# Kernel optimization log

Measured on AMD Instinct MI355X. Metric: run time of the kernel, lower is better.

Reference implementation:

```python
import math
import jax, jax.numpy as jnp
import numpy as np

D = 1024        # latent_dim
H = 16          # num latent heads
HD = D // H     # head dim = 64
T_EMB = 9       # max(diffusion_steps+1, 2)
CLIP = 1.0      # latent_update_clip
LN_EPS = 1e-5


def layer_norm(x, g, b):
    m = jnp.mean(x, axis=-1, keepdims=True)
    v = jnp.mean(jnp.square(x - m), axis=-1, keepdims=True)
    return (x - m) * jax.lax.rsqrt(v + LN_EPS) * g + b


def setup_inputs() -> dict:
    key = jax.random.key(0)
    ks = jax.random.split(key, 10)
    B, S = 64, 64
    s = 0.02
    return {
        "latents": jax.random.normal(ks[0], (B, S, D), jnp.float32),
        "t_table": jax.random.normal(ks[1], (T_EMB, D), jnp.float32) * s,
        "attn_g": jnp.ones((D,), jnp.float32),
        "attn_b": jnp.zeros((D,), jnp.float32),
        "ffn_g": jnp.ones((D,), jnp.float32),
        "ffn_b": jnp.zeros((D,), jnp.float32),
        "Wq": jax.random.normal(ks[2], (D, D), jnp.float32) * s,
        "Wk": jax.random.normal(ks[3], (D, D), jnp.float32) * s,
        "Wv": jax.random.normal(ks[4], (D, D), jnp.float32) * s,
        "Wo": jax.random.normal(ks[5], (D, D), jnp.float32) * s,
        "Win": jax.random.normal(ks[6], (2 * D, D), jnp.float32) * s,
        "b_in": jnp.zeros((2 * D,), jnp.float32),
        "Wout": jax.random.normal(ks[7], (D, 2 * D), jnp.float32) * s,
        "b_out": jnp.zeros((D,), jnp.float32),
        "steps": 8,
    }


def _slot_attention(x, Wq, Wk, Wv, Wo):
    B, S, _ = x.shape
    scale = 1.0 / math.sqrt(HD)
    # torch Linear: y = x @ W.T ; weights stored (out, in)
    q = (x @ Wq.T).reshape(B, S, H, HD)
    k = (x @ Wk.T).reshape(B, S, H, HD)
    v = (x @ Wv.T).reshape(B, S, H, HD)
    scores = jnp.einsum("bqhd,bkhd->bhqk", q, k) * scale
    probs = jax.nn.softmax(scores, axis=-1)
    out = jnp.einsum("bhqk,bkhd->bqhd", probs, v).reshape(B, S, D)
    return out @ Wo.T


def reference(latents, t_table, attn_g, attn_b, ffn_g, ffn_b,
              Wq, Wk, Wv, Wo, Win, b_in, Wout, b_out, steps):
    h = latents
    for step in range(steps):
        step_id = min(step, T_EMB - 1)
        t_emb = t_table[step_id][None, None, :]          # [1,1,D]
        attn_update = _slot_attention(layer_norm(h + t_emb, attn_g, attn_b),
                                      Wq, Wk, Wv, Wo)
        ffn_in = layer_norm(h + t_emb + attn_update, ffn_g, ffn_b)
        ffn_update = jax.nn.silu(ffn_in @ Win.T + b_in) @ Wout.T + b_out
        update = attn_update + ffn_update
        unorm = jnp.maximum(jnp.linalg.norm(update, axis=-1, keepdims=True), 1e-6)
        update = update * jnp.minimum(CLIP / unorm, 1.0)
        h = h + update / steps
    return h
```

## Files before the change

kernel.cpp:

```cpp
#include <hip/hip_runtime.h>
#include <hip/hip_bf16.h>

typedef __attribute__((ext_vector_type(8))) short bf16x8;
typedef __attribute__((ext_vector_type(4))) float f32x4;
typedef __attribute__((ext_vector_type(4))) int i32x4;

static __device__ __forceinline__ short f2bf(float f) {
    __hip_bfloat16 h = __float2bfloat16(f);
    return __builtin_bit_cast(short, h);
}
static __device__ __forceinline__ float bf2f(short s) {
    unsigned u = ((unsigned)(unsigned short)s) << 16;
    return __builtin_bit_cast(float, u);
}

static __device__ __forceinline__ void gload_lds16(const short* g, short* l) {
    __builtin_amdgcn_global_load_lds((const __attribute__((address_space(1))) void*)g,
                                     (__attribute__((address_space(3))) void*)l, 16, 0, 0);
}

__global__ void convert_all_kernel(
    const float* __restrict__ Wq, const float* __restrict__ Wk, const float* __restrict__ Wv,
    const float* __restrict__ Wo, const float* __restrict__ Win, const float* __restrict__ Wout,
    short* __restrict__ wQKV, short* __restrict__ wO, short* __restrict__ wIn, short* __restrict__ wOut)
{
    const int M1 = 1024 * 1024;
    for (int i = blockIdx.x * blockDim.x + threadIdx.x; i < 8 * M1; i += gridDim.x * blockDim.x) {
        if (i < 3 * M1) {
            float v = (i < M1) ? Wq[i] : (i < 2 * M1) ? Wk[i - M1] : Wv[i - 2 * M1];
            wQKV[i] = f2bf(v);
        } else if (i < 4 * M1) {
            wO[i - 3 * M1] = f2bf(Wo[i - 3 * M1]);
        } else if (i < 6 * M1) {
            wIn[i - 4 * M1] = f2bf(Win[i - 4 * M1]);
        } else {
            wOut[i - 6 * M1] = f2bf(Wout[i - 6 * M1]);
        }
    }
}

__global__ __launch_bounds__(256) void first_ln_kernel(
    const float* __restrict__ latents, float* __restrict__ h,
    const float* __restrict__ trow,
    const float* __restrict__ g, const float* __restrict__ bb,
    short* __restrict__ out)
{
    const int row = blockIdx.x;
    const int tid = threadIdx.x;
    const int lane = tid & 63;
    const int wid = tid >> 6;
    __shared__ float red[4];
    const float* hr = latents + (size_t)row * 1024;
    float x[4];
    float s = 0.f;
    #pragma unroll
    for (int i = 0; i < 4; ++i) {
        int c = tid + i * 256;
        float hv = hr[c];
        h[(size_t)row * 1024 + c] = hv;
        x[i] = hv + trow[c]; s += x[i];
    }
    #pragma unroll
    for (int o = 32; o >= 1; o >>= 1) s += __shfl_xor(s, o, 64);
    if (lane == 0) red[wid] = s;
    __syncthreads();
    float mean = (red[0] + red[1] + red[2] + red[3]) * (1.0f / 1024.0f);
    __syncthreads();
    float s2 = 0.f;
    #pragma unroll
    for (int i = 0; i < 4; ++i) { float d = x[i] - mean; s2 += d * d; }
    #pragma unroll
    for (int o = 32; o >= 1; o >>= 1) s2 += __shfl_xor(s2, o, 64);
    if (lane == 0) red[wid] = s2;
    __syncthreads();
    float var = (red[0] + red[1] + red[2] + red[3]) * (1.0f / 1024.0f);
    float rstd = rsqrtf(var + 1e-5f);
    #pragma unroll
    for (int i = 0; i < 4; ++i) {
        int c = tid + i * 256;
        out[(size_t)row * 1024 + c] = f2bf((x[i] - mean) * rstd * g[c] + bb[c]);
    }
}

__global__ __launch_bounds__(256) void ln_kernel(
    const float* __restrict__ hsrc, const float* __restrict__ trow,
    const short* __restrict__ add,
    const float* __restrict__ g, const float* __restrict__ bb,
    short* __restrict__ out)
{
    const int row = blockIdx.x;
    const int tid = threadIdx.x;
    const int lane = tid & 63;
    const int wid = tid >> 6;
    __shared__ float red[4];
    const float* hr = hsrc + (size_t)row * 1024;
    float x[4];
    float s = 0.f;
    #pragma unroll
    for (int i = 0; i < 4; ++i) {
        int c = tid + i * 256;
        float v = hr[c] + trow[c];
        if (add) v += bf2f(add[(size_t)row * 1024 + c]);
        x[i] = v; s += v;
    }
    #pragma unroll
    for (int o = 32; o >= 1; o >>= 1) s += __shfl_xor(s, o, 64);
    if (lane == 0) red[wid] = s;
    __syncthreads();
    float mean = (red[0] + red[1] + red[2] + red[3]) * (1.0f / 1024.0f);
    __syncthreads();
    float s2 = 0.f;
    #pragma unroll
    for (int i = 0; i < 4; ++i) { float d = x[i] - mean; s2 += d * d; }
    #pragma unroll
    for (int o = 32; o >= 1; o >>= 1) s2 += __shfl_xor(s2, o, 64);
    if (lane == 0) red[wid] = s2;
    __syncthreads();
    float var = (red[0] + red[1] + red[2] + red[3]) * (1.0f / 1024.0f);
    float rstd = rsqrtf(var + 1e-5f);
    #pragma unroll
    for (int i = 0; i < 4; ++i) {
        int c = tid + i * 256;
        out[(size_t)row * 1024 + c] = f2bf((x[i] - mean) * rstd * g[c] + bb[c]);
    }
}

__global__ __launch_bounds__(256) void clipln_kernel(
    const short* __restrict__ upd, float* __restrict__ h,
    const float* __restrict__ trow,
    const float* __restrict__ g, const float* __restrict__ bb,
    short* __restrict__ out)
{
    const int row = blockIdx.x;
    const int tid = threadIdx.x;
    const int lane = tid & 63;
    const int wid = tid >> 6;
    __shared__ float red[4];
    const short* ur = upd + (size_t)row * 1024;
    float u[4], hn[4];
    float s = 0.f;
    #pragma unroll
    for (int i = 0; i < 4; ++i) { u[i] = bf2f(ur[tid + i * 256]); s += u[i] * u[i]; }
    #pragma unroll
    for (int o = 32; o >= 1; o >>= 1) s += __shfl_xor(s, o, 64);
    if (lane == 0) red[wid] = s;
    __syncthreads();
    float nrm = sqrtf(red[0] + red[1] + red[2] + red[3]);
    float scale = fminf(1.0f / fmaxf(nrm, 1e-6f), 1.0f) * 0.125f;
    __syncthreads();
    float sm = 0.f;
    #pragma unroll
    for (int i = 0; i < 4; ++i) {
        int c = tid + i * 256;
        hn[i] = h[(size_t)row * 1024 + c] + u[i] * scale;
        h[(size_t)row * 1024 + c] = hn[i];
        hn[i] += trow[c];
        sm += hn[i];
    }
    #pragma unroll
    for (int o = 32; o >= 1; o >>= 1) sm += __shfl_xor(sm, o, 64);
    if (lane == 0) red[wid] = sm;
    __syncthreads();
    float mean = (red[0] + red[1] + red[2] + red[3]) * (1.0f / 1024.0f);
    __syncthreads();
    float s2 = 0.f;
    #pragma unroll
    for (int i = 0; i < 4; ++i) { float d = hn[i] - mean; s2 += d * d; }
    #pragma unroll
    for (int o = 32; o >= 1; o >>= 1) s2 += __shfl_xor(s2, o, 64);
    if (lane == 0) red[wid] = s2;
    __syncthreads();
    float var = (red[0] + red[1] + red[2] + red[3]) * (1.0f / 1024.0f);
    float rstd = rsqrtf(var + 1e-5f);
    #pragma unroll
    for (int i = 0; i < 4; ++i) {
        int c = tid + i * 256;
        out[(size_t)row * 1024 + c] = f2bf((hn[i] - mean) * rstd * g[c] + bb[c]);
    }
}

template<int BM, int ACT, int ADD, int BIAS>
__global__ __launch_bounds__(512) void gemm_kernel(
    const short* __restrict__ A, const short* __restrict__ B,
    const float* __restrict__ bias, const short* __restrict__ addsrc,
    short* __restrict__ Cout, int M, int N, int K)
{
    const int nwg = gridDim.x * gridDim.y;
    const int orig = blockIdx.y * gridDim.x + blockIdx.x;
    const int swzid = (orig & 7) * (nwg >> 3) + (orig >> 3);
    const int bn = (swzid % gridDim.x) * 128;
    const int bm = (swzid / gridDim.x) * BM;

    __shared__ __align__(16) short As[BM * 64];
    __shared__ __align__(16) short Bs[128 * 64];
    const int tid = threadIdx.x;
    const int lane = tid & 63;
    const int wid = tid >> 6;
    const int l15 = lane & 15;
    const int l4 = lane >> 4;

    constexpr int MF = 2;
    constexpr int NF = (BM == 128) ? 4 : 2;
    const int rowbase = (BM == 128) ? (wid >> 1) * 32 : (wid >> 2) * 32;
    const int colbase = (BM == 128) ? (wid & 1) * 64 : (wid & 3) * 32;

    constexpr int ALOADS = BM * 8 / 512;

    f32x4 acc[MF][NF];
    #pragma unroll
    for (int m = 0; m < MF; ++m)
        #pragma unroll
        for (int n = 0; n < NF; ++n)
            acc[m][n] = (f32x4)(0.f);

    const int nt = K >> 6;
    for (int t = 0; t < nt; ++t) {
        const int k0 = t << 6;
        #pragma unroll
        for (int i = 0; i < ALOADS; ++i) {
            int slot = i * 512 + tid;
            int row = slot >> 3;
            int colb = (slot & 7) * 16;
            int swz = (row & 7) << 4;
            const short* g = A + (size_t)(bm + row) * K + k0 + ((colb ^ swz) >> 1);
            gload_lds16(g, (short*)((char*)As + slot * 16));
        }
        #pragma unroll
        for (int i = 0; i < 2; ++i) {
            int slot = i * 512 + tid;
            int row = slot >> 3;
            int colb = (slot & 7) * 16;
            int swz = (row & 7) << 4;
            const short* g = B + (size_t)(bn + row) * K + k0 + ((colb ^ swz) >> 1);
            gload_lds16(g, (short*)((char*)Bs + slot * 16));
        }
        __syncthreads();
        #pragma unroll
        for (int ks = 0; ks < 2; ++ks) {
            int kb = ks * 64 + l4 * 16;
            bf16x8 a[MF], b[NF];
            #pragma unroll
            for (int m = 0; m < MF; ++m) {
                int row = rowbase + m * 16 + l15;
                a[m] = *(const bf16x8*)((const char*)As + row * 128 + (kb ^ ((row & 7) << 4)));
            }
            #pragma unroll
            for (int n = 0; n < NF; ++n) {
                int row = colbase + n * 16 + l15;
                b[n] = *(const bf16x8*)((const char*)Bs + row * 128 + (kb ^ ((row & 7) << 4)));
            }
            #pragma unroll
            for (int m = 0; m < MF; ++m)
                #pragma unroll
                for (int n = 0; n < NF; ++n)
                    acc[m][n] = __builtin_amdgcn_mfma_f32_16x16x32_bf16(a[m], b[n], acc[m][n], 0, 0, 0);
        }
        __syncthreads();
    }

    #pragma unroll
    for (int m = 0; m < MF; ++m) {
        int row = bm + rowbase + m * 16 + l4 * 4;
        #pragma unroll
        for (int n = 0; n < NF; ++n) {
            int col = bn + colbase + n * 16 + l15;
            float bv = BIAS ? bias[col] : 0.f;
            #pragma unroll
            for (int r = 0; r < 4; ++r) {
                float v = acc[m][n][r] + bv;
                if (ACT) v = v / (1.f + __expf(-v));
                if (ADD) v += bf2f(addsrc[(size_t)(row + r) * N + col]);
                Cout[(size_t)(row + r) * N + col] = f2bf(v);
            }
        }
    }
}

__global__ __launch_bounds__(256) void attn_kernel(
    const short* __restrict__ qkv,
    short* __restrict__ ctx)
{
    const int blk = blockIdx.x;
    const int b = blk >> 4, hh = blk & 15;
    const int bs0 = b * 64;
    __shared__ __align__(16) short qs[64 * 64];
    __shared__ __align__(16) short ks_[64 * 64];
    __shared__ __align__(16) short vt[64 * 64];
    __shared__ __align__(16) short ps[64 * 64];
    const int tid = threadIdx.x;
    const int lane = tid & 63;
    const int wid = tid >> 6;
    const int l15 = lane & 15;
    const int l4 = lane >> 4;

    #pragma unroll
    for (int i = 0; i < 2; ++i) {
        int slot = i * 256 + tid;
        int row = slot >> 3;
        int colb = (slot & 7) * 16;
        int swz = (row & 7) << 4;
        const short* gq = qkv + (size_t)(bs0 + row) * 3072 + hh * 64 + (slot & 7) * 8;
        *(i32x4*)((char*)qs + row * 128 + (colb ^ swz)) = *(const i32x4*)gq;
        const short* gk = qkv + (size_t)(bs0 + row) * 3072 + 1024 + hh * 64 + (slot & 7) * 8;
        *(i32x4*)((char*)ks_ + row * 128 + (colb ^ swz)) = *(const i32x4*)gk;
        const short* gv = qkv + (size_t)(bs0 + row) * 3072 + 2048 + hh * 64 + (slot & 7) * 8;
        i32x4 vv = *(const i32x4*)gv;
        const short* ve = (const short*)&vv;
        #pragma unroll
        for (int j = 0; j < 8; ++j) {
            int d = (slot & 7) * 8 + j;
            *(short*)((char*)vt + d * 128 + ((row * 2) ^ ((d & 7) << 4))) = ve[j];
        }
    }
    __syncthreads();

    f32x4 sc[4];
    #pragma unroll
    for (int n = 0; n < 4; ++n) sc[n] = (f32x4)(0.f);
    #pragma unroll
    for (int ksz = 0; ksz < 2; ++ksz) {
        int kb = ksz * 64 + l4 * 16;
        int arow = wid * 16 + l15;
        bf16x8 af = *(const bf16x8*)((const char*)qs + arow * 128 + (kb ^ ((arow & 7) << 4)));
        #pragma unroll
        for (int n = 0; n < 4; ++n) {
            int brow = n * 16 + l15;
            bf16x8 bf = *(const bf16x8*)((const char*)ks_ + brow * 128 + (kb ^ ((brow & 7) << 4)));
            sc[n] = __builtin_amdgcn_mfma_f32_16x16x32_bf16(af, bf, sc[n], 0, 0, 0);
        }
    }
    float sm[4];
    #pragma unroll
    for (int r = 0; r < 4; ++r) {
        float m = -1e30f;
        #pragma unroll
        for (int n = 0; n < 4; ++n) { sc[n][r] *= 0.125f; m = fmaxf(m, sc[n][r]); }
        #pragma unroll
        for (int o = 1; o < 16; o <<= 1) m = fmaxf(m, __shfl_xor(m, o, 64));
        float s = 0.f;
        #pragma unroll
        for (int n = 0; n < 4; ++n) { sc[n][r] = __expf(sc[n][r] - m); s += sc[n][r]; }
        #pragma unroll
        for (int o = 1; o < 16; o <<= 1) s += __shfl_xor(s, o, 64);
        sm[r] = 1.f / s;
    }
    #pragma unroll
    for (int n = 0; n < 4; ++n)
        #pragma unroll
        for (int r = 0; r < 4; ++r) {
            int row = wid * 16 + l4 * 4 + r;
            int col = n * 16 + l15;
            *(short*)((char*)ps + row * 128 + ((col * 2) ^ ((row & 7) << 4))) = f2bf(sc[n][r] * sm[r]);
        }
    __syncthreads();

    f32x4 o[4];
    #pragma unroll
    for (int n = 0; n < 4; ++n) o[n] = (f32x4)(0.f);
    #pragma unroll
    for (int ksz = 0; ksz < 2; ++ksz) {
        int kb = ksz * 64 + l4 * 16;
        int arow = wid * 16 + l15;
        bf16x8 af = *(const bf16x8*)((const char*)ps + arow * 128 + (kb ^ ((arow & 7) << 4)));
        #pragma unroll
        for (int n = 0; n < 4; ++n) {
            int vrow = n * 16 + l15;
            bf16x8 bf = *(const bf16x8*)((const char*)vt + vrow * 128 + (kb ^ ((vrow & 7) << 4)));
            o[n] = __builtin_amdgcn_mfma_f32_16x16x32_bf16(af, bf, o[n], 0, 0, 0);
        }
    }
    #pragma unroll
    for (int n = 0; n < 4; ++n)
        #pragma unroll
        for (int r = 0; r < 4; ++r) {
            int row = wid * 16 + l4 * 4 + r;
            int col = n * 16 + l15;
            ctx[(size_t)(bs0 + row) * 1024 + hh * 64 + col] = f2bf(o[n][r]);
        }
}

__global__ __launch_bounds__(256) void clip_kernel(const short* __restrict__ upd, float* __restrict__ h) {
    const int row = blockIdx.x;
    const int tid = threadIdx.x;
    const int lane = tid & 63;
    const int wid = tid >> 6;
    __shared__ float red[4];
    const short* ur = upd + (size_t)row * 1024;
    float x[4];
    float s = 0.f;
    #pragma unroll
    for (int i = 0; i < 4; ++i) { x[i] = bf2f(ur[tid + i * 256]); s += x[i] * x[i]; }
    #pragma unroll
    for (int o = 32; o >= 1; o >>= 1) s += __shfl_xor(s, o, 64);
    if (lane == 0) red[wid] = s;
    __syncthreads();
    float nrm = sqrtf(red[0] + red[1] + red[2] + red[3]);
    float unorm = fmaxf(nrm, 1e-6f);
    float scale = fminf(1.0f / unorm, 1.0f) * 0.125f;
    #pragma unroll
    for (int i = 0; i < 4; ++i) {
        int c = tid + i * 256;
        h[(size_t)row * 1024 + c] += x[i] * scale;
    }
}

extern "C" void kernel_launch(void* const* d_in, const int* in_sizes, int n_in,
                              void* d_out, int out_size, void* d_ws, size_t ws_size,
                              hipStream_t stream) {
    const float* latents = (const float*)d_in[0];
    const float* t_table = (const float*)d_in[1];
    const float* attn_g  = (const float*)d_in[2];
    const float* attn_b  = (const float*)d_in[3];
    const float* ffn_g   = (const float*)d_in[4];
    const float* ffn_b   = (const float*)d_in[5];
    const float* Wq      = (const float*)d_in[6];
    const float* Wk      = (const float*)d_in[7];
    const float* Wv      = (const float*)d_in[8];
    const float* Wo      = (const float*)d_in[9];
    const float* Win     = (const float*)d_in[10];
    const float* b_in    = (const float*)d_in[11];
    const float* Wout    = (const float*)d_in[12];
    const float* b_out   = (const float*)d_in[13];

    char* ws = (char*)d_ws;
    size_t off = 0;
    auto alloc = [&](size_t bytes) { char* p = ws + off; off += (bytes + 255) & ~(size_t)255; return p; };
    short* wQKV = (short*)alloc((size_t)3072 * 1024 * 2);
    short* wO   = (short*)alloc((size_t)1024 * 1024 * 2);
    short* wIn  = (short*)alloc((size_t)2048 * 1024 * 2);
    short* wOut = (short*)alloc((size_t)1024 * 2048 * 2);
    short* xln  = (short*)alloc((size_t)4096 * 1024 * 2);
    short* qkv  = (short*)alloc((size_t)4096 * 3072 * 2);
    short* hidden = qkv;
    short* ctx  = (short*)alloc((size_t)4096 * 1024 * 2);
    short* au   = (short*)alloc((size_t)4096 * 1024 * 2);
    short* upd  = (short*)alloc((size_t)4096 * 1024 * 2);

    float* h = (float*)d_out;

    convert_all_kernel<<<2048, 256, 0, stream>>>(Wq, Wk, Wv, Wo, Win, Wout, wQKV, wO, wIn, wOut);
    first_ln_kernel<<<4096, 256, 0, stream>>>(latents, h, t_table, attn_g, attn_b, xln);

    for (int step = 0; step < 8; ++step) {
        const float* trow = t_table + (size_t)step * 1024;
        gemm_kernel<128, 0, 0, 0><<<dim3(24, 32), 512, 0, stream>>>(xln, wQKV, nullptr, nullptr, qkv, 4096, 3072, 1024);
        attn_kernel<<<1024, 256, 0, stream>>>(qkv, ctx);
        gemm_kernel<64, 0, 0, 0><<<dim3(8, 64), 512, 0, stream>>>(ctx, wO, nullptr, nullptr, au, 4096, 1024, 1024);
        ln_kernel<<<4096, 256, 0, stream>>>(h, trow, au, ffn_g, ffn_b, xln);
        gemm_kernel<64, 1, 0, 1><<<dim3(16, 64), 512, 0, stream>>>(xln, wIn, b_in, nullptr, hidden, 4096, 2048, 1024);
        gemm_kernel<64, 0, 1, 1><<<dim3(8, 64), 512, 0, stream>>>(hidden, wOut, b_out, au, upd, 4096, 1024, 2048);
        if (step < 7) {
            clipln_kernel<<<4096, 256, 0, stream>>>(upd, h, t_table + (size_t)(step + 1) * 1024,
                                                    attn_g, attn_b, xln);
        } else {
            clip_kernel<<<4096, 256, 0, stream>>>(upd, h);
        }
    }
}
```

Measured before the change: 1.041 ms.

## Fuse QKV projection GEMM with per-head attention into one kernel

Replaces the separate QKV GEMM and attention kernels with a single kernel in which each block computes the 64x192 Q/K/V tile for one batch and head, then runs softmax attention straight from LDS. This removes the write and re-read of the 4096x3072 qkv intermediate and one kernel launch per step. In exchange, each block uses a small 64-row tile with 256 threads and no double buffering, so the GEMM part may run at lower MFMA efficiency. The A tile is also reloaded by all 16 head blocks of a batch.

```diff
diff --git a/kernel.cpp b/kernel.cpp
--- a/kernel.cpp
+++ b/kernel.cpp
@@ -179,6 +179,173 @@
     }
 }
 
+__global__ __launch_bounds__(256) void qkvattn_kernel(
+    const short* __restrict__ A,
+    const short* __restrict__ Bw,
+    short* __restrict__ ctx)
+{
+    const int nwg = gridDim.x;
+    const int orig = blockIdx.x;
+    const int swzid = (orig & 7) * (nwg >> 3) + (orig >> 3);
+    const int hh = swzid >> 6;
+    const int b  = swzid & 63;
+    const int bs0 = b * 64;
+
+    __shared__ __align__(16) short As[64 * 64];
+    __shared__ __align__(16) short Bs[192 * 64];
+    __shared__ __align__(16) short qs[64 * 64];
+    __shared__ __align__(16) short ks_[64 * 64];
+    __shared__ __align__(16) short vt[64 * 64];
+
+    const int tid = threadIdx.x;
+    const int lane = tid & 63;
+    const int wid = tid >> 6;
+    const int l15 = lane & 15;
+    const int l4 = lane >> 4;
+
+    f32x4 acc[4][3];
+    #pragma unroll
+    for (int m = 0; m < 4; ++m)
+        #pragma unroll
+        for (int n = 0; n < 3; ++n)
+            acc[m][n] = (f32x4)(0.f);
+
+    for (int t = 0; t < 16; ++t) {
+        const int k0 = t << 6;
+        #pragma unroll
+        for (int i = 0; i < 2; ++i) {
+            int slot = i * 256 + tid;
+            int row = slot >> 3;
+            int colb = (slot & 7) * 16;
+            int swz = (row & 7) << 4;
+            const short* g = A + (size_t)(bs0 + row) * 1024 + k0 + ((colb ^ swz) >> 1);
+            gload_lds16(g, (short*)((char*)As + slot * 16));
+        }
+        #pragma unroll
+        for (int i = 0; i < 6; ++i) {
+            int slot = i * 256 + tid;
+            int row = slot >> 3;
+            int colb = (slot & 7) * 16;
+            int swz = (row & 7) << 4;
+            int grow = ((row >> 6) << 10) + hh * 64 + (row & 63);
+            const short* g = Bw + (size_t)grow * 1024 + k0 + ((colb ^ swz) >> 1);
+            gload_lds16(g, (short*)((char*)Bs + slot * 16));
+        }
+        __syncthreads();
+        #pragma unroll
+        for (int ks = 0; ks < 2; ++ks) {
+            int kb = ks * 64 + l4 * 16;
+            bf16x8 a[4], bfr[3];
+            #pragma unroll
+            for (int m = 0; m < 4; ++m) {
+                int row = m * 16 + l15;
+                a[m] = *(const bf16x8*)((const char*)As + row * 128 + (kb ^ ((row & 7) << 4)));
+            }
+            #pragma unroll
+            for (int n = 0; n < 3; ++n) {
+                int row = (wid * 3 + n) * 16 + l15;
+                bfr[n] = *(const bf16x8*)((const char*)Bs + row * 128 + (kb ^ ((row & 7) << 4)));
+            }
+            #pragma unroll
+            for (int m = 0; m < 4; ++m)
+                #pragma unroll
+                for (int n = 0; n < 3; ++n)
+                    acc[m][n] = __builtin_amdgcn_mfma_f32_16x16x32_bf16(a[m], bfr[n], acc[m][n], 0, 0, 0);
+        }
+        __syncthreads();
+    }
+
+    #pragma unroll
+    for (int n = 0; n < 3; ++n) {
+        int cg = wid * 3 + n;
+        #pragma unroll
+        for (int m = 0; m < 4; ++m) {
+            #pragma unroll
+            for (int r = 0; r < 4; ++r) {
+                int row = m * 16 + l4 * 4 + r;
+                int col = cg * 16 + l15;
+                short v = f2bf(acc[m][n][r]);
+                if (cg < 4) {
+                    *(short*)((char*)qs + row * 128 + ((col * 2) ^ ((row & 7) << 4))) = v;
+                } else if (cg < 8) {
+                    int c = col - 64;
+                    *(short*)((char*)ks_ + row * 128 + ((c * 2) ^ ((row & 7) << 4))) = v;
+                } else {
+                    int d = col - 128;
+                    *(short*)((char*)vt + d * 128 + ((row * 2) ^ ((d & 7) << 4))) = v;
+                }
+            }
+        }
+    }
+    __syncthreads();
+
+    short* ps = As;
+
+    f32x4 sc[4];
+    #pragma unroll
+    for (int n = 0; n < 4; ++n) sc[n] = (f32x4)(0.f);
+    #pragma unroll
+    for (int ksz = 0; ksz < 2; ++ksz) {
+        int kb = ksz * 64 + l4 * 16;
+        int arow = wid * 16 + l15;
+        bf16x8 af = *(const bf16x8*)((const char*)qs + arow * 128 + (kb ^ ((arow & 7) << 4)));
+        #pragma unroll
+        for (int n = 0; n < 4; ++n) {
+            int brow = n * 16 + l15;
+            bf16x8 bf = *(const bf16x8*)((const char*)ks_ + brow * 128 + (kb ^ ((brow & 7) << 4)));
+            sc[n] = __builtin_amdgcn_mfma_f32_16x16x32_bf16(af, bf, sc[n], 0, 0, 0);
+        }
+    }
+    float sm[4];
+    #pragma unroll
+    for (int r = 0; r < 4; ++r) {
+        float m = -1e30f;
+        #pragma unroll
+        for (int n = 0; n < 4; ++n) { sc[n][r] *= 0.125f; m = fmaxf(m, sc[n][r]); }
+        #pragma unroll
+        for (int o = 1; o < 16; o <<= 1) m = fmaxf(m, __shfl_xor(m, o, 64));
+        float s = 0.f;
+        #pragma unroll
+        for (int n = 0; n < 4; ++n) { sc[n][r] = __expf(sc[n][r] - m); s += sc[n][r]; }
+        #pragma unroll
+        for (int o = 1; o < 16; o <<= 1) s += __shfl_xor(s, o, 64);
+        sm[r] = 1.f / s;
+    }
+    #pragma unroll
+    for (int n = 0; n < 4; ++n)
+        #pragma unroll
+        for (int r = 0; r < 4; ++r) {
+            int row = wid * 16 + l4 * 4 + r;
+            int col = n * 16 + l15;
+            *(short*)((char*)ps + row * 128 + ((col * 2) ^ ((row & 7) << 4))) = f2bf(sc[n][r] * sm[r]);
+        }
+    __syncthreads();
+
+    f32x4 o[4];
+    #pragma unroll
+    for (int n = 0; n < 4; ++n) o[n] = (f32x4)(0.f);
+    #pragma unroll
+    for (int ksz = 0; ksz < 2; ++ksz) {
+        int kb = ksz * 64 + l4 * 16;
+        int arow = wid * 16 + l15;
+        bf16x8 af = *(const bf16x8*)((const char*)ps + arow * 128 + (kb ^ ((arow & 7) << 4)));
+        #pragma unroll
+        for (int n = 0; n < 4; ++n) {
+            int vrow = n * 16 + l15;
+            bf16x8 bf = *(const bf16x8*)((const char*)vt + vrow * 128 + (kb ^ ((vrow & 7) << 4)));
+            o[n] = __builtin_amdgcn_mfma_f32_16x16x32_bf16(af, bf, o[n], 0, 0, 0);
+        }
+    }
+    #pragma unroll
+    for (int n = 0; n < 4; ++n)
+        #pragma unroll
+        for (int r = 0; r < 4; ++r) {
+            int row = wid * 16 + l4 * 4 + r;
+            int col = n * 16 + l15;
+            ctx[(size_t)(bs0 + row) * 1024 + hh * 64 + col] = f2bf(o[n][r]);
+        }
+}
+
 template<int BM, int ACT, int ADD, int BIAS>
 __global__ __launch_bounds__(512) void gemm_kernel(
     const short* __restrict__ A, const short* __restrict__ B,
@@ -274,109 +441,6 @@
             }
         }
     }
-}
-
-__global__ __launch_bounds__(256) void attn_kernel(
-    const short* __restrict__ qkv,
-    short* __restrict__ ctx)
-{
-    const int blk = blockIdx.x;
-    const int b = blk >> 4, hh = blk & 15;
-    const int bs0 = b * 64;
-    __shared__ __align__(16) short qs[64 * 64];
-    __shared__ __align__(16) short ks_[64 * 64];
-    __shared__ __align__(16) short vt[64 * 64];
-    __shared__ __align__(16) short ps[64 * 64];
-    const int tid = threadIdx.x;
-    const int lane = tid & 63;
-    const int wid = tid >> 6;
-    const int l15 = lane & 15;
-    const int l4 = lane >> 4;
-
-    #pragma unroll
-    for (int i = 0; i < 2; ++i) {
-        int slot = i * 256 + tid;
-        int row = slot >> 3;
-        int colb = (slot & 7) * 16;
-        int swz = (row & 7) << 4;
-        const short* gq = qkv + (size_t)(bs0 + row) * 3072 + hh * 64 + (slot & 7) * 8;
-        *(i32x4*)((char*)qs + row * 128 + (colb ^ swz)) = *(const i32x4*)gq;
-        const short* gk = qkv + (size_t)(bs0 + row) * 3072 + 1024 + hh * 64 + (slot & 7) * 8;
-        *(i32x4*)((char*)ks_ + row * 128 + (colb ^ swz)) = *(const i32x4*)gk;
-        const short* gv = qkv + (size_t)(bs0 + row) * 3072 + 2048 + hh * 64 + (slot & 7) * 8;
-        i32x4 vv = *(const i32x4*)gv;
-        const short* ve = (const short*)&vv;
-        #pragma unroll
-        for (int j = 0; j < 8; ++j) {
-            int d = (slot & 7) * 8 + j;
-            *(short*)((char*)vt + d * 128 + ((row * 2) ^ ((d & 7) << 4))) = ve[j];
-        }
-    }
-    __syncthreads();
-
-    f32x4 sc[4];
-    #pragma unroll
-    for (int n = 0; n < 4; ++n) sc[n] = (f32x4)(0.f);
-    #pragma unroll
-    for (int ksz = 0; ksz < 2; ++ksz) {
-        int kb = ksz * 64 + l4 * 16;
-        int arow = wid * 16 + l15;
-        bf16x8 af = *(const bf16x8*)((const char*)qs + arow * 128 + (kb ^ ((arow & 7) << 4)));
-        #pragma unroll
-        for (int n = 0; n < 4; ++n) {
-            int brow = n * 16 + l15;
-            bf16x8 bf = *(const bf16x8*)((const char*)ks_ + brow * 128 + (kb ^ ((brow & 7) << 4)));
-            sc[n] = __builtin_amdgcn_mfma_f32_16x16x32_bf16(af, bf, sc[n], 0, 0, 0);
-        }
-    }
-    float sm[4];
-    #pragma unroll
-    for (int r = 0; r < 4; ++r) {
-        float m = -1e30f;
-        #pragma unroll
-        for (int n = 0; n < 4; ++n) { sc[n][r] *= 0.125f; m = fmaxf(m, sc[n][r]); }
-        #pragma unroll
-        for (int o = 1; o < 16; o <<= 1) m = fmaxf(m, __shfl_xor(m, o, 64));
-        float s = 0.f;
-        #pragma unroll
-        for (int n = 0; n < 4; ++n) { sc[n][r] = __expf(sc[n][r] - m); s += sc[n][r]; }
-        #pragma unroll
-        for (int o = 1; o < 16; o <<= 1) s += __shfl_xor(s, o, 64);
-        sm[r] = 1.f / s;
-    }
-    #pragma unroll
-    for (int n = 0; n < 4; ++n)
-        #pragma unroll
-        for (int r = 0; r < 4; ++r) {
-            int row = wid * 16 + l4 * 4 + r;
-            int col = n * 16 + l15;
-            *(short*)((char*)ps + row * 128 + ((col * 2) ^ ((row & 7) << 4))) = f2bf(sc[n][r] * sm[r]);
-        }
-    __syncthreads();
-
-    f32x4 o[4];
-    #pragma unroll
-    for (int n = 0; n < 4; ++n) o[n] = (f32x4)(0.f);
-    #pragma unroll
-    for (int ksz = 0; ksz < 2; ++ksz) {
-        int kb = ksz * 64 + l4 * 16;
-        int arow = wid * 16 + l15;
-        bf16x8 af = *(const bf16x8*)((const char*)ps + arow * 128 + (kb ^ ((arow & 7) << 4)));
-        #pragma unroll
-        for (int n = 0; n < 4; ++n) {
-            int vrow = n * 16 + l15;
-            bf16x8 bf = *(const bf16x8*)((const char*)vt + vrow * 128 + (kb ^ ((vrow & 7) << 4)));
-            o[n] = __builtin_amdgcn_mfma_f32_16x16x32_bf16(af, bf, o[n], 0, 0, 0);
-        }
-    }
-    #pragma unroll
-    for (int n = 0; n < 4; ++n)
-        #pragma unroll
-        for (int r = 0; r < 4; ++r) {
-            int row = wid * 16 + l4 * 4 + r;
-            int col = n * 16 + l15;
-            ctx[(size_t)(bs0 + row) * 1024 + hh * 64 + col] = f2bf(o[n][r]);
-        }
 }
 
 __global__ __launch_bounds__(256) void clip_kernel(const short* __restrict__ upd, float* __restrict__ h) {
@@ -430,8 +494,7 @@
     short* wIn  = (short*)alloc((size_t)2048 * 1024 * 2);
     short* wOut = (short*)alloc((size_t)1024 * 2048 * 2);
     short* xln  = (short*)alloc((size_t)4096 * 1024 * 2);
-    short* qkv  = (short*)alloc((size_t)4096 * 3072 * 2);
-    short* hidden = qkv;
+    short* hidden = (short*)alloc((size_t)4096 * 2048 * 2);
     short* ctx  = (short*)alloc((size_t)4096 * 1024 * 2);
     short* au   = (short*)alloc((size_t)4096 * 1024 * 2);
     short* upd  = (short*)alloc((size_t)4096 * 1024 * 2);
@@ -443,8 +506,7 @@
 
     for (int step = 0; step < 8; ++step) {
         const float* trow = t_table + (size_t)step * 1024;
-        gemm_kernel<128, 0, 0, 0><<<dim3(24, 32), 512, 0, stream>>>(xln, wQKV, nullptr, nullptr, qkv, 4096, 3072, 1024);
-        attn_kernel<<<1024, 256, 0, stream>>>(qkv, ctx);
+        qkvattn_kernel<<<1024, 256, 0, stream>>>(xln, wQKV, ctx);
         gemm_kernel<64, 0, 0, 0><<<dim3(8, 64), 512, 0, stream>>>(ctx, wO, nullptr, nullptr, au, 4096, 1024, 1024);
         ln_kernel<<<4096, 256, 0, stream>>>(h, trow, au, ffn_g, ffn_b, xln);
         gemm_kernel<64, 1, 0, 1><<<dim3(16, 64), 512, 0, stream>>>(xln, wIn, b_in, nullptr, hidden, 4096, 2048, 1024);
```

Measured after the change: 1.092 ms. 4.9% more time.
